# Kernel optimization log

Hardware: AMD Instinct MI355X
Metric: run time of the kernel (lower is better)

## Reference

```python
import jax, jax.numpy as jnp
import numpy as np

N_HEAD = 16  # matches init_kwargs
LN_EPS = 1e-5


def setup_inputs() -> dict:
    key = jax.random.key(0)
    k0, k1, k2 = jax.random.split(key, 3)
    S, B, D = 2048, 2, 1024
    N, Dh = N_HEAD, D // N_HEAD
    h = jax.random.normal(k0, (S, B, D), dtype=jnp.float32)
    # causal mask, True = masked; source's dim==3 branch: shape [qlen, klen, batch]
    causal = jnp.triu(jnp.ones((S, S), dtype=bool), k=1)
    attn_mask = jnp.broadcast_to(causal[:, :, None], (S, S, B))
    W_qkv = jax.random.normal(k1, (D, 3 * N * Dh), dtype=jnp.float32) * (1.0 / np.sqrt(D))
    W_o = jax.random.normal(k2, (N * Dh, D), dtype=jnp.float32) * (1.0 / np.sqrt(N * Dh))
    gamma = jnp.ones((D,), dtype=jnp.float32)
    beta = jnp.zeros((D,), dtype=jnp.float32)
    return {"h": h, "attn_mask": attn_mask, "W_qkv": W_qkv, "W_o": W_o,
            "gamma": gamma, "beta": beta}


def reference(h, attn_mask, W_qkv, W_o, gamma, beta):
    # h: [S, B, D] (seq, batch, d_model) -- Transformer-XL layout
    S, B, D = h.shape
    N = N_HEAD
    Dh = W_o.shape[0] // N
    scale = 1.0 / np.sqrt(Dh)

    qkv = h @ W_qkv                                   # [S, B, 3*N*Dh]
    q, k, v = jnp.split(qkv, 3, axis=-1)
    q = q.reshape(S, B, N, Dh)
    k = k.reshape(S, B, N, Dh)
    v = v.reshape(S, B, N, Dh)

    # attention scores: [i, j, b, n]
    score = jnp.einsum('ibnd,jbnd->ijbn', q, k) * scale
    # mask (dim==3 branch of source): attn_mask [i, j, b] -> [i, j, b, 1]
    score = jnp.where(attn_mask[:, :, :, None], -jnp.inf, score)
    prob = jax.nn.softmax(score, axis=1)              # softmax over key axis j

    attn_vec = jnp.einsum('ijbn,jbnd->ibnd', prob, v).reshape(S, B, N * Dh)
    attn_out = attn_vec @ W_o                         # [S, B, D]

    # residual + LayerNorm (biased variance, like torch.nn.LayerNorm)
    x = h + attn_out
    mu = jnp.mean(x, axis=-1, keepdims=True)
    var = jnp.mean(jnp.square(x - mu), axis=-1, keepdims=True)
    out = (x - mu) * jax.lax.rsqrt(var + LN_EPS) * gamma + beta
    return out
```

## Files before the change

kernel.cpp:

```cpp
#include <hip/hip_runtime.h>

typedef unsigned short u16;
typedef unsigned int u32;
typedef __attribute__((ext_vector_type(8))) __bf16 bf16x8;
typedef __attribute__((ext_vector_type(4))) float f32x4;
typedef __attribute__((ext_vector_type(16))) float f32x16;
typedef __attribute__((ext_vector_type(8))) unsigned short u16x8;
typedef __attribute__((ext_vector_type(4))) unsigned short u16x4;
typedef __attribute__((ext_vector_type(2))) unsigned int u32x2;
typedef __attribute__((ext_vector_type(4))) unsigned int u32x4;

__device__ __forceinline__ u16 f2bf(float f) {
    u32 u = __builtin_bit_cast(u32, f);
    u += 0x7fffu + ((u >> 16) & 1u);
    return (u16)(u >> 16);
}

__device__ __forceinline__ float fexp2(float x) {
#if __has_builtin(__builtin_amdgcn_exp2f)
    return __builtin_amdgcn_exp2f(x);
#else
    return exp2f(x);
#endif
}

__device__ __forceinline__ float frcp(float x) {
#if __has_builtin(__builtin_amdgcn_rcpf)
    return __builtin_amdgcn_rcpf(x);
#else
    return 1.0f / x;
#endif
}

__global__ __launch_bounds__(256) void conv_h_kernel(const float* __restrict__ h,
                                                     u16* __restrict__ hb) {
    int i = blockIdx.x * 256 + threadIdx.x;
    float4 v = ((const float4*)h)[i];
    u16x4 o = { f2bf(v.x), f2bf(v.y), f2bf(v.z), f2bf(v.w) };
    ((u16x4*)hb)[i] = o;
}

__global__ __launch_bounds__(256) void conv_wt_kernel(const float* __restrict__ W,
                                                      u16* __restrict__ Wt,
                                                      int R, int C,
                                                      int scale_rows, float scale) {
    __shared__ float tile[32][33];
    int t = threadIdx.x;
    int r = t >> 3, c4 = (t & 7) * 4;
    int gx = blockIdx.x * 32, gy = blockIdx.y * 32;
    float4 v = *(const float4*)&W[(size_t)(gy + r) * C + gx + c4];
    tile[r][c4 + 0] = v.x; tile[r][c4 + 1] = v.y;
    tile[r][c4 + 2] = v.z; tile[r][c4 + 3] = v.w;
    __syncthreads();
    float sc = (gx + r < scale_rows) ? scale : 1.0f;
    u16x4 o = { f2bf(tile[c4 + 0][r] * sc), f2bf(tile[c4 + 1][r] * sc),
                f2bf(tile[c4 + 2][r] * sc), f2bf(tile[c4 + 3][r] * sc) };
    *(u16x4*)&Wt[(size_t)(gx + r) * R + gy + c4] = o;
}

template <int MODE>
__global__ __launch_bounds__(256) void gemm_bt_kernel(
        const u16* __restrict__ A, const u16* __restrict__ Bt,
        u16* __restrict__ Cb, const float* __restrict__ H, float* __restrict__ X,
        int M, int N, int K) {
    constexpr int LDT = 40;
    __shared__ u16 alds[2][128 * LDT];
    __shared__ u16 blds[2][128 * LDT];
    const int t = threadIdx.x;
    const int lane = t & 63;
    const int wave = t >> 6;
    const int wm = wave >> 1, wn = wave & 1;
    const int m0 = blockIdx.x * 128;
    const int n0 = blockIdx.y * 128;
    const int nk = K >> 5;

    const int srow = t >> 1;
    const int sch = (t & 1) * 2;
    const u16* ga = A + (size_t)(m0 + srow) * K + sch * 8;
    const u16* gb = Bt + (size_t)(n0 + srow) * K + sch * 8;
    const int wo = srow * LDT + sch * 8;

    u16x8 ra0 = *(const u16x8*)(ga);
    u16x8 ra1 = *(const u16x8*)(ga + 8);
    u16x8 rb0 = *(const u16x8*)(gb);
    u16x8 rb1 = *(const u16x8*)(gb + 8);
    *(u16x8*)&alds[0][wo] = ra0;  *(u16x8*)&alds[0][wo + 8] = ra1;
    *(u16x8*)&blds[0][wo] = rb0;  *(u16x8*)&blds[0][wo + 8] = rb1;

    f32x4 acc[4][4] = {};
    const int ko = (lane >> 4) * 8;
    const int arow_base = wm * 64 + (lane & 15);
    const int brow_base = wn * 64 + (lane & 15);

    int cur = 0;
    for (int kt = 0; kt < nk; ++kt) {
        __syncthreads();
        if (kt + 1 < nk) {
            const u16* gan = ga + (kt + 1) * 32;
            const u16* gbn = gb + (kt + 1) * 32;
            ra0 = *(const u16x8*)(gan);
            ra1 = *(const u16x8*)(gan + 8);
            rb0 = *(const u16x8*)(gbn);
            rb1 = *(const u16x8*)(gbn + 8);
        }
        bf16x8 afrag[4], bfrag[4];
#pragma unroll
        for (int m = 0; m < 4; ++m)
            afrag[m] = *(const bf16x8*)&alds[cur][(arow_base + m * 16) * LDT + ko];
#pragma unroll
        for (int n = 0; n < 4; ++n)
            bfrag[n] = *(const bf16x8*)&blds[cur][(brow_base + n * 16) * LDT + ko];
#pragma unroll
        for (int m = 0; m < 4; ++m)
#pragma unroll
            for (int n = 0; n < 4; ++n)
                acc[m][n] = __builtin_amdgcn_mfma_f32_16x16x32_bf16(afrag[m], bfrag[n],
                                                                   acc[m][n], 0, 0, 0);
        if (kt + 1 < nk) {
            *(u16x8*)&alds[cur ^ 1][wo] = ra0;  *(u16x8*)&alds[cur ^ 1][wo + 8] = ra1;
            *(u16x8*)&blds[cur ^ 1][wo] = rb0;  *(u16x8*)&blds[cur ^ 1][wo + 8] = rb1;
        }
        cur ^= 1;
    }

#pragma unroll
    for (int m = 0; m < 4; ++m)
#pragma unroll
        for (int n = 0; n < 4; ++n)
#pragma unroll
            for (int r = 0; r < 4; ++r) {
                int row = m0 + wm * 64 + m * 16 + (lane >> 4) * 4 + r;
                int col = n0 + wn * 64 + n * 16 + (lane & 15);
                size_t idx = (size_t)row * N + col;
                if (MODE == 0) Cb[idx] = f2bf(acc[m][n][r]);
                else           X[idx] = acc[m][n][r] + H[idx];
            }
}

__global__ __launch_bounds__(256) void transpose_v_kernel(const u16* __restrict__ qkvb,
                                                          u16* __restrict__ vt) {
    __shared__ u16 tl[64][72];
    const int t = threadIdx.x;
    const int p = blockIdx.y;
    const int nn = p >> 1, b = p & 1;
    const int s0 = blockIdx.x * 64;
    const int r = t >> 2;
    const int ch = (t & 3) * 2;
    const u16* g = qkvb + ((size_t)(s0 + r) * 2 + b) * 3072 + 2048 + nn * 64;
    *(u16x8*)&tl[r][ch * 8]     = *(const u16x8*)(g + ch * 8);
    *(u16x8*)&tl[r][ch * 8 + 8] = *(const u16x8*)(g + ch * 8 + 8);
    __syncthreads();
    const int dh = t >> 2;
    const int sc = (t & 3) * 2;
    u16* o = vt + ((size_t)p * 64 + dh) * 2048 + s0;
#pragma unroll
    for (int q = 0; q < 2; ++q) {
        int scq = sc + q;
        u16x8 v;
#pragma unroll
        for (int j = 0; j < 8; ++j) v[j] = tl[scq * 8 + j][dh];
        *(u16x8*)(o + scq * 8) = v;
    }
}

__global__ __launch_bounds__(512, 4) void attn_kernel(const u16* __restrict__ qkvb,
                                                      const u16* __restrict__ vt,
                                                      u16* __restrict__ attnb) {
    constexpr int LKT = 72;
    __shared__ u16 kvs[2][2][2][64 * LKT];
    const int t = threadIdx.x;
    const int lane = t & 63;
    const int w = (t >> 6) & 3;
    const int grp = t >> 8;
    const int bid = blockIdx.x;
    const int g = bid >> 5;
    const int qt = (g < 8) ? (15 - g) : (g - 8);
    const int p = bid & 31;
    const int nn = p >> 1, b = p & 1;
    const int i0 = qt * 128;

    const int il = lane & 31;
    const int hi = lane >> 5;

    bf16x8 qa[4];
    {
        const u16* qg = qkvb + ((size_t)(i0 + w * 32 + il) * 2 + b) * 3072
                        + nn * 64 + hi * 8;
#pragma unroll
        for (int kc = 0; kc < 4; ++kc)
            qa[kc] = *(const bf16x8*)(qg + kc * 16);
    }

    f32x16 o[2] = {};
    float mrun = -3.0e38f;
    float lrun = 0.f;

    const int tg = t & 255;
    const int srow = tg >> 2;
    const int sch = (tg & 3) * 2;
    const u16* kg = qkvb + 1024 + nn * 64 + sch * 8;
    const u16* vg = vt + ((size_t)p * 64 + srow) * 2048 + sch * 8;
    const int swo = srow * LKT + sch * 8;

    const int nt = 2 * qt + 2;
    const int G = nt >> 1;

    u16x8 k0, k1, v0, v1;
    {
        const u16* kgp = kg + ((size_t)(grp * 64 + srow) * 2 + b) * 3072;
        k0 = *(const u16x8*)(kgp);  k1 = *(const u16x8*)(kgp + 8);
        const u16* vgp = vg + grp * 64;
        v0 = *(const u16x8*)(vgp);  v1 = *(const u16x8*)(vgp + 8);
        *(u16x8*)&kvs[grp][0][0][swo] = k0;  *(u16x8*)&kvs[grp][0][0][swo + 8] = k1;
        *(u16x8*)&kvs[grp][0][1][swo] = v0;  *(u16x8*)&kvs[grp][0][1][swo + 8] = v1;
    }
    __syncthreads();

    for (int s = 0; s < G; ++s) {
        const int jt = 2 * s + grp;
        const int buf = s & 1;
        if (jt + 2 < nt) {
            const u16* kgp = kg + ((size_t)((jt + 2) * 64 + srow) * 2 + b) * 3072;
            k0 = *(const u16x8*)(kgp);  k1 = *(const u16x8*)(kgp + 8);
            const u16* vgp = vg + (jt + 2) * 64;
            v0 = *(const u16x8*)(vgp);  v1 = *(const u16x8*)(vgp + 8);
        }

        const bool skip = (jt * 64 > i0 + w * 32 + 31);
        if (!skip) {
            const u16* kl = &kvs[grp][buf][0][0];
            const u16* vl = &kvs[grp][buf][1][0];

            f32x16 st[2];
            __builtin_amdgcn_s_setprio(1);
#pragma unroll
            for (int jc = 0; jc < 2; ++jc) {
                f32x16 z = {};
#pragma unroll
                for (int kc = 0; kc < 4; ++kc) {
                    bf16x8 kb = *(const bf16x8*)&kl[(jc * 32 + il) * LKT + kc * 16 + hi * 8];
                    z = __builtin_amdgcn_mfma_f32_32x32x16_bf16(kb, qa[kc], z, 0, 0, 0);
                }
                st[jc] = z;
            }
            __builtin_amdgcn_s_setprio(0);

            if (jt * 64 + 63 > i0 + w * 32) {
                const int iglob = i0 + w * 32 + il;
#pragma unroll
                for (int jc = 0; jc < 2; ++jc)
#pragma unroll
                    for (int r = 0; r < 16; ++r) {
                        int jglob = jt * 64 + jc * 32 + (r & 3) + 8 * (r >> 2) + 4 * hi;
                        if (jglob > iglob) st[jc][r] = -3.0e38f;
                    }
            }

            float mloc = st[0][0];
#pragma unroll
            for (int jc = 0; jc < 2; ++jc)
#pragma unroll
                for (int r = 0; r < 16; ++r) mloc = fmaxf(mloc, st[jc][r]);
            mloc = fmaxf(mloc, __shfl_xor(mloc, 32, 64));

            if (__any(mloc > mrun + 8.0f)) {
                float mnew = fmaxf(mrun, mloc);
                float alpha = fexp2(mrun - mnew);
                lrun *= alpha;
                mrun = mnew;
#pragma unroll
                for (int r = 0; r < 16; ++r) {
                    float ar = __shfl(alpha, (r & 3) + 8 * (r >> 2) + 4 * hi, 64);
                    o[0][r] *= ar;
                    o[1][r] *= ar;
                }
            }

            float rsum = 0.f;
#pragma unroll
            for (int jc = 0; jc < 2; ++jc) {
                u32 W[4][2];
#pragma unroll
                for (int gg = 0; gg < 4; ++gg)
#pragma unroll
                    for (int u = 0; u < 2; ++u) {
                        float p0 = fexp2(st[jc][4 * gg + 2 * u] - mrun);
                        float p1 = fexp2(st[jc][4 * gg + 2 * u + 1] - mrun);
                        rsum += p0 + p1;
                        u32 wres;
                        asm("v_cvt_pk_bf16_f32 %0, %1, %2" : "=v"(wres) : "v"(p0), "v"(p1));
                        W[gg][u] = wres;
                    }
                __builtin_amdgcn_s_setprio(1);
#pragma unroll
                for (int jk = 0; jk < 2; ++jk) {
                    u32x2 s0 = __builtin_amdgcn_permlane32_swap(W[2 * jk][0], W[2 * jk + 1][0], false, false);
                    u32x2 s1 = __builtin_amdgcn_permlane32_swap(W[2 * jk][1], W[2 * jk + 1][1], false, false);
                    u32x4 fw = { s0[0], s1[0], s0[1], s1[1] };
                    bf16x8 pa = __builtin_bit_cast(bf16x8, fw);
#pragma unroll
                    for (int cf = 0; cf < 2; ++cf) {
                        bf16x8 vb = *(const bf16x8*)&vl[(cf * 32 + il) * LKT
                                                        + jc * 32 + jk * 16 + hi * 8];
                        o[cf] = __builtin_amdgcn_mfma_f32_32x32x16_bf16(pa, vb, o[cf], 0, 0, 0);
                    }
                }
                __builtin_amdgcn_s_setprio(0);
            }
            rsum += __shfl_xor(rsum, 32, 64);
            lrun += rsum;
        }

        if (jt + 2 < nt) {
            *(u16x8*)&kvs[grp][buf ^ 1][0][swo] = k0;  *(u16x8*)&kvs[grp][buf ^ 1][0][swo + 8] = k1;
            *(u16x8*)&kvs[grp][buf ^ 1][1][swo] = v0;  *(u16x8*)&kvs[grp][buf ^ 1][1][swo + 8] = v1;
        }
        __syncthreads();
    }

    float* osc = (float*)&kvs[1][0][0][0];
    float* msc = osc + 128 * 65;
    float* lsc = msc + 128;
    if (grp == 1) {
#pragma unroll
        for (int cf = 0; cf < 2; ++cf)
#pragma unroll
            for (int r = 0; r < 16; ++r) {
                int iL = (r & 3) + 8 * (r >> 2) + 4 * hi;
                osc[(w * 32 + iL) * 65 + cf * 32 + il] = o[cf][r];
            }
        if (hi == 0) { msc[w * 32 + il] = mrun; lsc[w * 32 + il] = lrun; }
    }
    __syncthreads();
    if (grp == 0) {
        float mB = msc[w * 32 + il];
        float lB = lsc[w * 32 + il];
        float m = fmaxf(mrun, mB);
        float eA = fexp2(mrun - m);
        float eB = fexp2(mB - m);
        float linv = frcp(lrun * eA + lB * eB);
#pragma unroll
        for (int r = 0; r < 16; ++r) {
            int iL = (r & 3) + 8 * (r >> 2) + 4 * hi;
            float eAr = __shfl(eA, iL, 64);
            float eBr = __shfl(eB, iL, 64);
            float rvr = __shfl(linv, iL, 64);
            int row = i0 + w * 32 + iL;
            u16* og = attnb + ((size_t)row * 2 + b) * 1024 + nn * 64;
#pragma unroll
            for (int cf = 0; cf < 2; ++cf) {
                float ob = osc[(w * 32 + iL) * 65 + cf * 32 + il];
                og[cf * 32 + il] = f2bf((o[cf][r] * eAr + ob * eBr) * rvr);
            }
        }
    }
}

__global__ __launch_bounds__(256) void ln_kernel(const float* __restrict__ X,
                                                 const float* __restrict__ gamma,
                                                 const float* __restrict__ beta,
                                                 float* __restrict__ out) {
    __shared__ float red[8];
    const int t = threadIdx.x;
    const int row = blockIdx.x;
    float4 v = ((const float4*)(X + (size_t)row * 1024))[t];
    float s = v.x + v.y + v.z + v.w;
#pragma unroll
    for (int off = 1; off < 64; off <<= 1) s += __shfl_xor(s, off, 64);
    if ((t & 63) == 0) red[t >> 6] = s;
    __syncthreads();
    float mu = (red[0] + red[1] + red[2] + red[3]) * (1.f / 1024.f);
    float dx = v.x - mu, dy = v.y - mu, dz = v.z - mu, dw = v.w - mu;
    float q = dx * dx + dy * dy + dz * dz + dw * dw;
#pragma unroll
    for (int off = 1; off < 64; off <<= 1) q += __shfl_xor(q, off, 64);
    if ((t & 63) == 0) red[4 + (t >> 6)] = q;
    __syncthreads();
    float var = (red[4] + red[5] + red[6] + red[7]) * (1.f / 1024.f);
    float rs = rsqrtf(var + 1e-5f);
    float4 g = ((const float4*)gamma)[t];
    float4 bt = ((const float4*)beta)[t];
    float4 o;
    o.x = dx * rs * g.x + bt.x;
    o.y = dy * rs * g.y + bt.y;
    o.z = dz * rs * g.z + bt.z;
    o.w = dw * rs * g.w + bt.w;
    ((float4*)(out + (size_t)row * 1024))[t] = o;
}

extern "C" void kernel_launch(void* const* d_in, const int* in_sizes, int n_in,
                              void* d_out, int out_size, void* d_ws, size_t ws_size,
                              hipStream_t stream) {
    const float* h     = (const float*)d_in[0];
    const float* Wqkv  = (const float*)d_in[2];
    const float* Wo    = (const float*)d_in[3];
    const float* gamma = (const float*)d_in[4];
    const float* beta  = (const float*)d_in[5];
    float* out = (float*)d_out;

    char* ws = (char*)d_ws;
    u16*   hb    = (u16*)(ws);
    u16*   wqkvt = (u16*)(ws + 8388608);
    u16*   wot   = (u16*)(ws + 14680064);
    u16*   qkvb  = (u16*)(ws + 16777216);
    u16*   vt    = (u16*)(ws + 41943040);
    u16*   attnb = (u16*)(ws + 50331648);
    float* xbuf  = (float*)(ws + 58720256);

    const float qscale = 0.125f * 1.44269504088896f;

    conv_h_kernel<<<4096, 256, 0, stream>>>(h, hb);
    conv_wt_kernel<<<dim3(96, 32), 256, 0, stream>>>(Wqkv, wqkvt, 1024, 3072, 1024, qscale);
    conv_wt_kernel<<<dim3(32, 32), 256, 0, stream>>>(Wo, wot, 1024, 1024, 0, 1.0f);
    gemm_bt_kernel<0><<<dim3(32, 24), 256, 0, stream>>>(hb, wqkvt, qkvb, nullptr, nullptr,
                                                        4096, 3072, 1024);
    transpose_v_kernel<<<dim3(32, 32), 256, 0, stream>>>(qkvb, vt);
    attn_kernel<<<512, 512, 0, stream>>>(qkvb, vt, attnb);
    gemm_bt_kernel<1><<<dim3(32, 8), 256, 0, stream>>>(attnb, wot, nullptr, h, xbuf,
                                                       4096, 1024, 1024);
    ln_kernel<<<4096, 256, 0, stream>>>(xbuf, gamma, beta, out);
}
```

Baseline: 122.9 us.

## Drop split-KV wave groups in attention; single group iterates all key tiles

The attention kernel previously used 512 threads split into two groups, each covering alternate key tiles, and merged their partial softmax results through shared memory at the end. It now uses 256 threads (one group of 4 waves) that walk every key tile sequentially with a double-buffered K/V prefetch, which removes the cross-group merge, its LDS traffic and extra barrier, and halves the shared memory footprint. The trade-off is less intra-block parallelism: each wave does twice as many serial tiles, so latency hiding relies on more resident blocks per CU.

```diff
diff --git a/kernel.cpp b/kernel.cpp
--- a/kernel.cpp
+++ b/kernel.cpp
@@ -163,15 +163,14 @@
     }
 }
 
-__global__ __launch_bounds__(512, 4) void attn_kernel(const u16* __restrict__ qkvb,
+__global__ __launch_bounds__(256, 4) void attn_kernel(const u16* __restrict__ qkvb,
                                                       const u16* __restrict__ vt,
                                                       u16* __restrict__ attnb) {
     constexpr int LKT = 72;
-    __shared__ u16 kvs[2][2][2][64 * LKT];
+    __shared__ u16 kvs[2][2][64 * LKT];
     const int t = threadIdx.x;
     const int lane = t & 63;
-    const int w = (t >> 6) & 3;
-    const int grp = t >> 8;
+    const int w = t >> 6;
     const int bid = blockIdx.x;
     const int g = bid >> 5;
     const int qt = (g < 8) ? (15 - g) : (g - 8);
@@ -195,41 +194,36 @@
     float mrun = -3.0e38f;
     float lrun = 0.f;
 
-    const int tg = t & 255;
-    const int srow = tg >> 2;
-    const int sch = (tg & 3) * 2;
+    const int srow = t >> 2;
+    const int sch = (t & 3) * 2;
     const u16* kg = qkvb + 1024 + nn * 64 + sch * 8;
     const u16* vg = vt + ((size_t)p * 64 + srow) * 2048 + sch * 8;
     const int swo = srow * LKT + sch * 8;
 
     const int nt = 2 * qt + 2;
-    const int G = nt >> 1;
-
     u16x8 k0, k1, v0, v1;
     {
-        const u16* kgp = kg + ((size_t)(grp * 64 + srow) * 2 + b) * 3072;
+        const u16* kgp = kg + ((size_t)srow * 2 + b) * 3072;
         k0 = *(const u16x8*)(kgp);  k1 = *(const u16x8*)(kgp + 8);
-        const u16* vgp = vg + grp * 64;
-        v0 = *(const u16x8*)(vgp);  v1 = *(const u16x8*)(vgp + 8);
-        *(u16x8*)&kvs[grp][0][0][swo] = k0;  *(u16x8*)&kvs[grp][0][0][swo + 8] = k1;
-        *(u16x8*)&kvs[grp][0][1][swo] = v0;  *(u16x8*)&kvs[grp][0][1][swo + 8] = v1;
-    }
-    __syncthreads();
-
-    for (int s = 0; s < G; ++s) {
-        const int jt = 2 * s + grp;
-        const int buf = s & 1;
-        if (jt + 2 < nt) {
-            const u16* kgp = kg + ((size_t)((jt + 2) * 64 + srow) * 2 + b) * 3072;
+        v0 = *(const u16x8*)(vg);   v1 = *(const u16x8*)(vg + 8);
+    }
+    *(u16x8*)&kvs[0][0][swo] = k0;  *(u16x8*)&kvs[0][0][swo + 8] = k1;
+    *(u16x8*)&kvs[0][1][swo] = v0;  *(u16x8*)&kvs[0][1][swo + 8] = v1;
+    __syncthreads();
+
+    for (int jt = 0; jt < nt; ++jt) {
+        const int buf = jt & 1;
+        if (jt + 1 < nt) {
+            const u16* kgp = kg + ((size_t)((jt + 1) * 64 + srow) * 2 + b) * 3072;
             k0 = *(const u16x8*)(kgp);  k1 = *(const u16x8*)(kgp + 8);
-            const u16* vgp = vg + (jt + 2) * 64;
+            const u16* vgp = vg + (jt + 1) * 64;
             v0 = *(const u16x8*)(vgp);  v1 = *(const u16x8*)(vgp + 8);
         }
 
         const bool skip = (jt * 64 > i0 + w * 32 + 31);
         if (!skip) {
-            const u16* kl = &kvs[grp][buf][0][0];
-            const u16* vl = &kvs[grp][buf][1][0];
+            const u16* kl = &kvs[buf][0][0];
+            const u16* vl = &kvs[buf][1][0];
 
             f32x16 st[2];
             __builtin_amdgcn_s_setprio(1);
@@ -311,48 +305,23 @@
             lrun += rsum;
         }
 
-        if (jt + 2 < nt) {
-            *(u16x8*)&kvs[grp][buf ^ 1][0][swo] = k0;  *(u16x8*)&kvs[grp][buf ^ 1][0][swo + 8] = k1;
-            *(u16x8*)&kvs[grp][buf ^ 1][1][swo] = v0;  *(u16x8*)&kvs[grp][buf ^ 1][1][swo + 8] = v1;
+        if (jt + 1 < nt) {
+            *(u16x8*)&kvs[buf ^ 1][0][swo] = k0;  *(u16x8*)&kvs[buf ^ 1][0][swo + 8] = k1;
+            *(u16x8*)&kvs[buf ^ 1][1][swo] = v0;  *(u16x8*)&kvs[buf ^ 1][1][swo + 8] = v1;
         }
         __syncthreads();
     }
 
-    float* osc = (float*)&kvs[1][0][0][0];
-    float* msc = osc + 128 * 65;
-    float* lsc = msc + 128;
-    if (grp == 1) {
+    float rinv = frcp(lrun);
+#pragma unroll
+    for (int r = 0; r < 16; ++r) {
+        int iL = (r & 3) + 8 * (r >> 2) + 4 * hi;
+        float rvr = __shfl(rinv, iL, 64);
+        int row = i0 + w * 32 + iL;
+        u16* og = attnb + ((size_t)row * 2 + b) * 1024 + nn * 64;
 #pragma unroll
         for (int cf = 0; cf < 2; ++cf)
-#pragma unroll
-            for (int r = 0; r < 16; ++r) {
-                int iL = (r & 3) + 8 * (r >> 2) + 4 * hi;
-                osc[(w * 32 + iL) * 65 + cf * 32 + il] = o[cf][r];
-            }
-        if (hi == 0) { msc[w * 32 + il] = mrun; lsc[w * 32 + il] = lrun; }
-    }
-    __syncthreads();
-    if (grp == 0) {
-        float mB = msc[w * 32 + il];
-        float lB = lsc[w * 32 + il];
-        float m = fmaxf(mrun, mB);
-        float eA = fexp2(mrun - m);
-        float eB = fexp2(mB - m);
-        float linv = frcp(lrun * eA + lB * eB);
-#pragma unroll
-        for (int r = 0; r < 16; ++r) {
-            int iL = (r & 3) + 8 * (r >> 2) + 4 * hi;
-            float eAr = __shfl(eA, iL, 64);
-            float eBr = __shfl(eB, iL, 64);
-            float rvr = __shfl(linv, iL, 64);
-            int row = i0 + w * 32 + iL;
-            u16* og = attnb + ((size_t)row * 2 + b) * 1024 + nn * 64;
-#pragma unroll
-            for (int cf = 0; cf < 2; ++cf) {
-                float ob = osc[(w * 32 + iL) * 65 + cf * 32 + il];
-                og[cf * 32 + il] = f2bf((o[cf][r] * eAr + ob * eBr) * rvr);
-            }
-        }
+            og[cf * 32 + il] = f2bf(o[cf][r] * rvr);
     }
 }
 
@@ -415,7 +384,7 @@
     gemm_bt_kernel<0><<<dim3(32, 24), 256, 0, stream>>>(hb, wqkvt, qkvb, nullptr, nullptr,
                                                         4096, 3072, 1024);
     transpose_v_kernel<<<dim3(32, 32), 256, 0, stream>>>(qkvb, vt);
-    attn_kernel<<<512, 512, 0, stream>>>(qkvb, vt, attnb);
+    attn_kernel<<<512, 256, 0, stream>>>(qkvb, vt, attnb);
     gemm_bt_kernel<1><<<dim3(32, 8), 256, 0, stream>>>(attnb, wot, nullptr, h, xbuf,
                                                        4096, 1024, 1024);
     ln_kernel<<<4096, 256, 0, stream>>>(xbuf, gamma, beta, out);
```

Measured after the change: 135.2 us. 1.1x slower.
